# Kernel tuning notes

Measured on AMD Instinct MI355X. Metric: run time of the kernel, lower is better.

Reference implementation:

```python
import jax, jax.numpy as jnp
import numpy as np

KSIZE = 7
SIGMA = 3.0
ALPHA = 0.1
POS_VAL_FOR_ALL_NEG = 5.0
NEG_VAL_FOR_ALL_POS = -5.0


def _gauss_kernel():
    x = jnp.arange(KSIZE, dtype=jnp.float32) - (KSIZE - 1) / 2.0
    pdf = jnp.exp(-0.5 * (x / SIGMA) ** 2)
    return pdf / pdf.sum()


def _gaussian_blur(img):
    # img: (B, C, H, W); separable 7x7 gaussian, reflect padding (torchvision behavior)
    B, C, H, W = img.shape
    k = _gauss_kernel()
    pad = KSIZE // 2
    x = jnp.pad(img, ((0, 0), (0, 0), (pad, pad), (pad, pad)), mode='reflect')
    x = x.reshape(B * C, 1, H + 2 * pad, W + 2 * pad)
    kh = k.reshape(1, 1, KSIZE, 1)
    kw = k.reshape(1, 1, 1, KSIZE)
    x = jax.lax.conv_general_dilated(x, kh, (1, 1), 'VALID')
    x = jax.lax.conv_general_dilated(x, kw, (1, 1), 'VALID')
    return x.reshape(B, C, H, W)


def _dup_map(x, mask, fallback):
    # x, mask: (L,). Gather x[mask] (original order) then tile to length L.
    # Stable argsort puts True(=selected) positions first in original order.
    L = x.shape[0]
    cnt = mask.sum()
    order = jnp.argsort(jnp.logical_not(mask))  # selected indices first, stable
    idx = order[jnp.arange(L) % jnp.maximum(cnt, 1)]
    return jnp.where(cnt == 0, jnp.float32(fallback), x[idx])


_dup_vmapped = jax.vmap(_dup_map, in_axes=(0, 0, None))


def _bce_with_logits(x, y):
    # mean( max(x,0) - x*y + log1p(exp(-|x|)) ) == mean( softplus(x) - x*y )
    return jnp.mean(jnp.logaddexp(0.0, x) - x * y)


def _forward(inp, tgt):
    B, C, H, W = inp.shape
    aug_sim_target = (_gaussian_blur(tgt * 255.0) > 0).astype(jnp.float32)

    L = H * W
    x = inp.reshape(B * C, L)
    t = tgt.reshape(B * C, L)
    a = aug_sim_target.reshape(B * C, L)

    # duplicated_pos: gather input at target>0, tile; fallback +5 if no positives
    pos_mask = t > 0
    dup_pos = _dup_vmapped(x, pos_mask, POS_VAL_FOR_ALL_NEG)

    # duplicated_false_pos: prefer (input>0 & ~aug_pos); else all negatives; else -5
    aug_pos = a > 0
    fp_mask = jnp.logical_and(x > 0, jnp.logical_not(aug_pos))
    neg_mask = jnp.logical_not(aug_pos)
    cnt_fp = fp_mask.sum(axis=1, keepdims=True)
    chosen_mask = jnp.where(cnt_fp > 0, fp_mask, neg_mask)
    dup_fp = _dup_vmapped(x, chosen_mask, NEG_VAL_FOR_ALL_POS)

    sim = dup_pos * x
    aug_sim = dup_pos * dup_fp

    sim_loss = _bce_with_logits(sim, t) + _bce_with_logits(dup_pos, jnp.ones_like(x))
    aug_sim_loss = _bce_with_logits(aug_sim, jnp.zeros_like(x))
    return sim_loss + ALPHA * aug_sim_loss


def setup_inputs() -> dict:
    key = jax.random.key(0)
    k1, k2 = jax.random.split(key)
    B, C, H, W = 16, 3, 512, 512
    inp = jax.random.normal(k1, (B, C, H, W), dtype=jnp.float32)
    tgt = jax.random.randint(k2, (B, C, H, W), 0, 2).astype(jnp.float32)
    return {"input": inp, "target": tgt}


def reference(input, target):
    return _forward(input, target)
```

## Files before the change

### kernel.cpp

```cpp
#include <hip/hip_runtime.h>
#include <math.h>

constexpr int W = 512;
constexpr int HIMG = 512;
constexpr int L = 1 << 18;
constexpr int LOG2L = 18;
constexpr int TPB = 256;
constexpr int TPB1 = 512;
constexpr int TILE = 2048;
constexpr int TILES_PER_ROW = L / TILE;
constexpr int WORDS_PER_TILE = TILE / 64;
constexpr int SPB = 16;
constexpr int HALO = 3;
constexpr int HBUF = SPB + 2 * HALO;
constexpr int BLK_PER_IMG = HIMG / SPB;
constexpr int LBLK = 32;
constexpr int LOG2LBLK = 5;
constexpr int CHUNK = L / LBLK;
constexpr int LIT = CHUNK / (TPB * 4);

typedef unsigned long long ull;

__device__ __forceinline__ float softplus_f(float v) {
    return fmaxf(v, 0.0f) +
           0.6931471805599453f *
               __builtin_amdgcn_logf(1.0f + __builtin_amdgcn_exp2f(-fabsf(v) * 1.4426950408889634f));
}

__device__ __forceinline__ ull hdil7(ull prev, ull cur, ull next) {
    ull r = cur;
    r |= (cur >> 1) | (next << 63);
    r |= (cur >> 2) | (next << 62);
    r |= (cur >> 3) | (next << 61);
    r |= (cur << 1) | (prev >> 63);
    r |= (cur << 2) | (prev >> 62);
    r |= (cur << 3) | (prev >> 61);
    return r;
}

template <typename T>
__device__ __forceinline__ T sel8(const T* a, int k) {
    return k == 0 ? a[0] : k == 1 ? a[1] : k == 2 ? a[2] : k == 3 ? a[3]
         : k == 4 ? a[4] : k == 5 ? a[5] : k == 6 ? a[6] : a[7];
}

__global__ __launch_bounds__(TPB1)
void fused_mask_kernel(const float* __restrict__ x, const float* __restrict__ t,
                       ull* __restrict__ mT, ull* __restrict__ mFp, ull* __restrict__ mNeg,
                       int* __restrict__ cPos, int* __restrict__ cFp, int* __restrict__ cNeg) {
    int b = blockIdx.x;
    int img = b >> 5;
    int y0 = (b & 31) * SPB;
    int gs0 = img * HIMG + y0;

    __shared__ ull hbuf[HBUF][8];
    __shared__ ull tbuf[SPB][8];
    __shared__ ull xbuf[SPB][8];

    int lane = threadIdx.x & 63;
    int wv = threadIdx.x >> 6;
    int ylo = (y0 - HALO < 0) ? 0 : y0 - HALO;
    int yhi = (y0 + SPB - 1 + HALO > HIMG - 1) ? HIMG - 1 : y0 + SPB - 1 + HALO;

    for (int yl = ylo + wv; yl <= yhi; yl += 8) {
        int gbase = (img * HIMG + yl) * W;
        bool own = (yl >= y0) && (yl < y0 + SPB);
        ull wt[8], wx[8], h[8];
#pragma unroll
        for (int k = 0; k < 8; ++k) wt[k] = __ballot(t[gbase + k * 64 + lane] > 0.0f);
        if (own) {
#pragma unroll
            for (int k = 0; k < 8; ++k) wx[k] = __ballot(x[gbase + k * 64 + lane] > 0.0f);
        }
#pragma unroll
        for (int k = 0; k < 8; ++k) {
            ull cur = wt[k];
            ull prev = k ? wt[k - 1]
                         : ((((cur >> 1) & 1ull) << 63) | (((cur >> 2) & 1ull) << 62) |
                            (((cur >> 3) & 1ull) << 61));
            ull next = (k < 7) ? wt[k + 1]
                               : (((cur >> 62) & 1ull) | (((cur >> 61) & 1ull) << 1) |
                                  (((cur >> 60) & 1ull) << 2));
            h[k] = hdil7(prev, cur, next);
        }
        int hy = yl - (y0 - HALO);
        int k = lane & 7;
        if (lane < 8) {
            hbuf[hy][k] = sel8(h, k);
        } else if (own && lane < 16) {
            tbuf[yl - y0][k] = sel8(wt, k);
            mT[(img * HIMG + yl) * 8 + k] = sel8(wt, k);
        } else if (own && lane < 24) {
            xbuf[yl - y0][k] = sel8(wx, k);
        }
    }
    __syncthreads();

    int tid = threadIdx.x;
    if (tid < SPB * 8) {
        int ys = tid >> 3;
        int c = tid & 7;
        int y = y0 + ys;
        ull wa = 0;
#pragma unroll
        for (int d = -3; d <= 3; ++d) {
            int yy = y + d;
            yy = yy < 0 ? -yy : (yy > HIMG - 1 ? 2 * (HIMG - 1) - yy : yy);
            wa |= hbuf[yy - (y0 - HALO)][c];
        }
        ull tw = tbuf[ys][c];
        ull fp = xbuf[ys][c] & ~wa;
        ull ng = ~wa;
        int gw = gs0 * 8 + tid;
        mFp[gw] = fp;
        mNeg[gw] = ng;
        int pT = __popcll(tw), pF = __popcll(fp), pN = __popcll(ng);
#pragma unroll
        for (int m = 1; m < 32; m <<= 1) {
            pT += __shfl_xor(pT, m, 64);
            pF += __shfl_xor(pF, m, 64);
            pN += __shfl_xor(pN, m, 64);
        }
        if ((lane & 31) == 0) {
            int tile = img * TILES_PER_ROW + (y0 >> 2) + (tid >> 5);
            cPos[tile] = pT; cFp[tile] = pF; cNeg[tile] = pN;
        }
    }
}

__global__ void scan_kernel(const int* __restrict__ cPos, const int* __restrict__ cFp,
                            const int* __restrict__ cNeg,
                            int* __restrict__ oPos, int* __restrict__ oCh,
                            int* __restrict__ rCp, int* __restrict__ rCc,
                            ull* __restrict__ rMp, ull* __restrict__ rMc,
                            int* __restrict__ rUseFp) {
    int r = blockIdx.x;
    int tid = threadIdx.x;
    __shared__ int ssp[TILES_PER_ROW], ssf[TILES_PER_ROW], ssn[TILES_PER_ROW];
    int myp = cPos[r * TILES_PER_ROW + tid];
    int myf = cFp[r * TILES_PER_ROW + tid];
    int myn = cNeg[r * TILES_PER_ROW + tid];
    ssp[tid] = myp; ssf[tid] = myf; ssn[tid] = myn;
    __syncthreads();
    for (int off = 1; off < TILES_PER_ROW; off <<= 1) {
        int ap = 0, af = 0, an = 0;
        if (tid >= off) { ap = ssp[tid - off]; af = ssf[tid - off]; an = ssn[tid - off]; }
        __syncthreads();
        if (tid >= off) { ssp[tid] += ap; ssf[tid] += af; ssn[tid] += an; }
        __syncthreads();
    }
    int cp = ssp[TILES_PER_ROW - 1], cf = ssf[TILES_PER_ROW - 1], cn = ssn[TILES_PER_ROW - 1];
    bool useFp = cf > 0;
    int tile = r * TILES_PER_ROW + tid;
    oPos[tile] = ssp[tid] - myp;
    oCh[tile] = useFp ? (ssf[tid] - myf) : (ssn[tid] - myn);
    if (tid == 0) {
        int cc = useFp ? cf : cn;
        rCp[r] = cp; rCc[r] = cc; rUseFp[r] = useFp ? 1 : 0;
        ull dp_ = (ull)(cp > 0 ? cp : 1);
        ull dc_ = (ull)(cc > 0 ? cc : 1);
        rMp[r] = ((1ull << 40) + dp_ - 1) / dp_;
        rMc[r] = ((1ull << 40) + dc_ - 1) / dc_;
    }
}

__global__ __launch_bounds__(TPB)
void scatter_kernel(const float* __restrict__ x, const ull* __restrict__ mT,
                    const ull* __restrict__ mFp, const ull* __restrict__ mNeg,
                    const int* __restrict__ oPos, const int* __restrict__ oCh,
                    const int* __restrict__ rUseFp,
                    float* __restrict__ xp, float* __restrict__ xf) {
    int tile = blockIdx.x;
    int tid = threadIdx.x;
    int lane = tid & 63;
    int wv = tid >> 6;
    int r = tile >> 7;
    bool useFp = rUseFp[r] != 0;
    int widx = tile * WORDS_PER_TILE + (tid >> 3);
    int shift = (tid & 7) * 8;
    unsigned bT = (unsigned)(mT[widx] >> shift) & 0xFF;
    ull chw = useFp ? mFp[widx] : mNeg[widx];
    unsigned bCh = (unsigned)(chw >> shift) & 0xFF;
    const float4* x4 = (const float4*)x;
    int b4 = tile * (TILE / 4) + tid * 2;
    float4 a = x4[b4], b = x4[b4 + 1];
    float xv[8] = {a.x, a.y, a.z, a.w, b.x, b.y, b.z, b.w};
    int p = __popc(bT), c = __popc(bCh);
    int v = p | (c << 16);
    int incl = v;
#pragma unroll
    for (int off = 1; off < 64; off <<= 1) {
        int n = __shfl_up(incl, off, 64);
        if (lane >= off) incl += n;
    }
    __shared__ int wtot[4];
    __shared__ float bufP[TILE], bufC[TILE];
    if (lane == 63) wtot[wv] = incl;
    __syncthreads();
    int base = 0;
    if (wv > 0) base += wtot[0];
    if (wv > 1) base += wtot[1];
    if (wv > 2) base += wtot[2];
    int tot = wtot[0] + wtot[1] + wtot[2] + wtot[3];
    int excl = base + incl - v;
    int ep = excl & 0xFFFF;
    int ec = (excl >> 16) & 0xFFFF;
#pragma unroll
    for (int e = 0; e < 8; ++e) {
        if ((bT >> e) & 1) bufP[ep++] = xv[e];
        if ((bCh >> e) & 1) bufC[ec++] = xv[e];
    }
    __syncthreads();
    int P = tot & 0xFFFF, C = (tot >> 16) & 0xFFFF;
    int rL = r << LOG2L;
    int pbase = rL + oPos[tile];
    for (int i = tid; i < P; i += TPB) xp[pbase + i] = bufP[i];
    int cbase = rL + oCh[tile];
    for (int i = tid; i < C; i += TPB) xf[cbase + i] = bufC[i];
}

__global__ __launch_bounds__(TPB)
void loss_kernel(const float* __restrict__ x, const ull* __restrict__ mT,
                 const float* __restrict__ xp, const float* __restrict__ xf,
                 const int* __restrict__ rCp, const int* __restrict__ rCc,
                 const ull* __restrict__ rMp, const ull* __restrict__ rMc,
                 double* __restrict__ partial) {
    int r = blockIdx.x >> LOG2LBLK;
    int cb = (blockIdx.x & (LBLK - 1)) * CHUNK;
    int rL = r << LOG2L;
    int cp = rCp[r], cc = rCc[r];
    ull Mp = rMp[r], Mc = rMc[r];
    const float4* x4 = (const float4*)(x + rL + cb);
    const float* xpr = xp + rL;
    const float* xfr = xf + rL;
    const ull* mtr = mT + (rL >> 6);
    float local = 0.0f;
#pragma unroll
    for (int it = 0; it < LIT; ++it) {
        int o4 = it * TPB + threadIdx.x;
        unsigned l = (unsigned)(cb + (o4 << 2));
        float4 xv = x4[o4];
        unsigned tb = (unsigned)(mtr[l >> 6] >> (l & 63)) & 0xFu;
        float dps[4], dfs[4];
        if (cp > 0) {
            unsigned d = (unsigned)cp;
            unsigned q = (unsigned)(((ull)l * Mp) >> 40);
            unsigned m0 = l - q * d;
            if ((int)m0 <= (int)d - 4) {
                float4 v;
                __builtin_memcpy(&v, xpr + m0, 16);
                dps[0] = v.x; dps[1] = v.y; dps[2] = v.z; dps[3] = v.w;
            } else {
                unsigned m1 = m0 + 1; if (m1 == d) m1 = 0;
                unsigned m2 = m1 + 1; if (m2 == d) m2 = 0;
                unsigned m3 = m2 + 1; if (m3 == d) m3 = 0;
                dps[0] = xpr[m0]; dps[1] = xpr[m1]; dps[2] = xpr[m2]; dps[3] = xpr[m3];
            }
        } else {
            dps[0] = dps[1] = dps[2] = dps[3] = 5.0f;
        }
        if (cc > 0) {
            unsigned d = (unsigned)cc;
            unsigned q = (unsigned)(((ull)l * Mc) >> 40);
            unsigned m0 = l - q * d;
            if ((int)m0 <= (int)d - 4) {
                float4 v;
                __builtin_memcpy(&v, xfr + m0, 16);
                dfs[0] = v.x; dfs[1] = v.y; dfs[2] = v.z; dfs[3] = v.w;
            } else {
                unsigned m1 = m0 + 1; if (m1 == d) m1 = 0;
                unsigned m2 = m1 + 1; if (m2 == d) m2 = 0;
                unsigned m3 = m2 + 1; if (m3 == d) m3 = 0;
                dfs[0] = xfr[m0]; dfs[1] = xfr[m1]; dfs[2] = xfr[m2]; dfs[3] = xfr[m3];
            }
        } else {
            dfs[0] = dfs[1] = dfs[2] = dfs[3] = -5.0f;
        }
        float xs[4] = {xv.x, xv.y, xv.z, xv.w};
#pragma unroll
        for (int k = 0; k < 4; ++k) {
            float sim = dps[k] * xs[k];
            float s1 = ((tb >> k) & 1) ? -sim : sim;
            local += softplus_f(s1) + softplus_f(-dps[k]) + 0.1f * softplus_f(dps[k] * dfs[k]);
        }
    }
    __shared__ double sd[TPB];
    int tid = threadIdx.x;
    sd[tid] = (double)local;
    __syncthreads();
    for (int off = TPB / 2; off > 0; off >>= 1) {
        if (tid < off) sd[tid] += sd[tid + off];
        __syncthreads();
    }
    if (tid == 0) partial[blockIdx.x] = sd[0];
}

__global__ __launch_bounds__(TPB)
void final_reduce(const double* __restrict__ partial, int n,
                  float* __restrict__ out, double inv_ntot) {
    __shared__ double sd[TPB];
    double s = 0.0;
    for (int i = threadIdx.x; i < n; i += TPB) s += partial[i];
    sd[threadIdx.x] = s;
    __syncthreads();
    for (int off = TPB / 2; off > 0; off >>= 1) {
        if (threadIdx.x < off) sd[threadIdx.x] += sd[threadIdx.x + off];
        __syncthreads();
    }
    if (threadIdx.x == 0) out[0] = (float)(sd[0] * inv_ntot);
}

extern "C" void kernel_launch(void* const* d_in, const int* in_sizes, int n_in,
                              void* d_out, int out_size, void* d_ws, size_t ws_size,
                              hipStream_t stream) {
    const float* x = (const float*)d_in[0];
    const float* t = (const float*)d_in[1];
    float* out = (float*)d_out;

    int ntot = in_sizes[0];
    int R = ntot >> LOG2L;
    int numTiles = ntot / TILE;
    int nwords = ntot / 64;
    int nMaskBlk = ntot / (SPB * W);
    int nLossBlk = R * LBLK;

    char* ws = (char*)d_ws;
    size_t off = 0;
    auto alloc = [&](size_t bytes) {
        size_t p = off;
        off = (off + bytes + 255) & ~(size_t)255;
        return (void*)(ws + p);
    };
    ull* mT   = (ull*)alloc((size_t)nwords * 8);
    ull* mFp  = (ull*)alloc((size_t)nwords * 8);
    ull* mNeg = (ull*)alloc((size_t)nwords * 8);
    int* cPos = (int*)alloc(numTiles * sizeof(int));
    int* cFp  = (int*)alloc(numTiles * sizeof(int));
    int* cNeg = (int*)alloc(numTiles * sizeof(int));
    int* oPos = (int*)alloc(numTiles * sizeof(int));
    int* oCh  = (int*)alloc(numTiles * sizeof(int));
    int* rCp = (int*)alloc(R * sizeof(int));
    int* rCc = (int*)alloc(R * sizeof(int));
    int* rUseFp = (int*)alloc(R * sizeof(int));
    ull* rMp = (ull*)alloc(R * sizeof(ull));
    ull* rMc = (ull*)alloc(R * sizeof(ull));
    double* partial = (double*)alloc((size_t)nLossBlk * sizeof(double));
    float* xp = (float*)alloc((size_t)ntot * sizeof(float));
    float* xf = (float*)alloc((size_t)ntot * sizeof(float));

    fused_mask_kernel<<<nMaskBlk, TPB1, 0, stream>>>(x, t, mT, mFp, mNeg, cPos, cFp, cNeg);
    scan_kernel<<<R, TILES_PER_ROW, 0, stream>>>(cPos, cFp, cNeg, oPos, oCh,
                                                 rCp, rCc, rMp, rMc, rUseFp);
    scatter_kernel<<<numTiles, TPB, 0, stream>>>(x, mT, mFp, mNeg, oPos, oCh, rUseFp, xp, xf);
    loss_kernel<<<nLossBlk, TPB, 0, stream>>>(x, mT, xp, xf, rCp, rCc, rMp, rMc, partial);
    final_reduce<<<1, TPB, 0, stream>>>(partial, nLossBlk, out, 1.0 / (double)ntot);
}
```

Before: 160.8 us.

## Fold per-row scan into scatter and loss kernels, drop scan launch

Removes the separate scan kernel. Each scatter block now recomputes its row's exclusive tile offsets and the fp-vs-neg choice from the 128 per-tile counts using wave shuffles. Each loss block likewise recomputes the row totals and magic divisors. This saves one launch and its intermediate buffers, at the cost of redundant small reductions in every block. The positive scatter write is also vectorised to 16-byte stores where possible, although the global destination may not be 16-byte aligned.

```diff
diff --git a/kernel.cpp b/kernel.cpp
--- a/kernel.cpp
+++ b/kernel.cpp
@@ -128,54 +128,46 @@
     }
 }
 
-__global__ void scan_kernel(const int* __restrict__ cPos, const int* __restrict__ cFp,
-                            const int* __restrict__ cNeg,
-                            int* __restrict__ oPos, int* __restrict__ oCh,
-                            int* __restrict__ rCp, int* __restrict__ rCc,
-                            ull* __restrict__ rMp, ull* __restrict__ rMc,
-                            int* __restrict__ rUseFp) {
-    int r = blockIdx.x;
-    int tid = threadIdx.x;
-    __shared__ int ssp[TILES_PER_ROW], ssf[TILES_PER_ROW], ssn[TILES_PER_ROW];
-    int myp = cPos[r * TILES_PER_ROW + tid];
-    int myf = cFp[r * TILES_PER_ROW + tid];
-    int myn = cNeg[r * TILES_PER_ROW + tid];
-    ssp[tid] = myp; ssf[tid] = myf; ssn[tid] = myn;
-    __syncthreads();
-    for (int off = 1; off < TILES_PER_ROW; off <<= 1) {
-        int ap = 0, af = 0, an = 0;
-        if (tid >= off) { ap = ssp[tid - off]; af = ssf[tid - off]; an = ssn[tid - off]; }
-        __syncthreads();
-        if (tid >= off) { ssp[tid] += ap; ssf[tid] += af; ssn[tid] += an; }
-        __syncthreads();
-    }
-    int cp = ssp[TILES_PER_ROW - 1], cf = ssf[TILES_PER_ROW - 1], cn = ssn[TILES_PER_ROW - 1];
-    bool useFp = cf > 0;
-    int tile = r * TILES_PER_ROW + tid;
-    oPos[tile] = ssp[tid] - myp;
-    oCh[tile] = useFp ? (ssf[tid] - myf) : (ssn[tid] - myn);
-    if (tid == 0) {
-        int cc = useFp ? cf : cn;
-        rCp[r] = cp; rCc[r] = cc; rUseFp[r] = useFp ? 1 : 0;
-        ull dp_ = (ull)(cp > 0 ? cp : 1);
-        ull dc_ = (ull)(cc > 0 ? cc : 1);
-        rMp[r] = ((1ull << 40) + dp_ - 1) / dp_;
-        rMc[r] = ((1ull << 40) + dc_ - 1) / dc_;
-    }
-}
-
 __global__ __launch_bounds__(TPB)
 void scatter_kernel(const float* __restrict__ x, const ull* __restrict__ mT,
                     const ull* __restrict__ mFp, const ull* __restrict__ mNeg,
-                    const int* __restrict__ oPos, const int* __restrict__ oCh,
-                    const int* __restrict__ rUseFp,
+                    const int* __restrict__ cPos, const int* __restrict__ cFp,
+                    const int* __restrict__ cNeg,
                     float* __restrict__ xp, float* __restrict__ xf) {
     int tile = blockIdx.x;
     int tid = threadIdx.x;
     int lane = tid & 63;
     int wv = tid >> 6;
     int r = tile >> 7;
-    bool useFp = rUseFp[r] != 0;
+    int tIdx = tile & 127;
+    int rowbase = r * TILES_PER_ROW;
+
+    int cpj = 0, cfj = 0, cnj = 0;
+    if (tid < TILES_PER_ROW) {
+        cpj = cPos[rowbase + tid];
+        cfj = cFp[rowbase + tid];
+        cnj = cNeg[rowbase + tid];
+    }
+    int totf = cfj;
+    int prep = (tid < tIdx) ? cpj : 0;
+    int pref = (tid < tIdx) ? cfj : 0;
+    int pren = (tid < tIdx) ? cnj : 0;
+#pragma unroll
+    for (int m = 1; m < 64; m <<= 1) {
+        totf += __shfl_xor(totf, m, 64);
+        prep += __shfl_xor(prep, m, 64);
+        pref += __shfl_xor(pref, m, 64);
+        pren += __shfl_xor(pren, m, 64);
+    }
+    __shared__ int red[4][4];
+    if (lane == 0) { red[wv][0] = totf; red[wv][1] = prep; red[wv][2] = pref; red[wv][3] = pren; }
+    __syncthreads();
+    int totF  = red[0][0] + red[1][0] + red[2][0] + red[3][0];
+    int oPosv = red[0][1] + red[1][1] + red[2][1] + red[3][1];
+    bool useFp = totF > 0;
+    int oChv = useFp ? (red[0][2] + red[1][2] + red[2][2] + red[3][2])
+                     : (red[0][3] + red[1][3] + red[2][3] + red[3][3]);
+
     int widx = tile * WORDS_PER_TILE + (tid >> 3);
     int shift = (tid & 7) * 8;
     unsigned bT = (unsigned)(mT[widx] >> shift) & 0xFF;
@@ -194,7 +186,8 @@
         if (lane >= off) incl += n;
     }
     __shared__ int wtot[4];
-    __shared__ float bufP[TILE], bufC[TILE];
+    __shared__ __align__(16) float bufP[TILE];
+    __shared__ __align__(16) float bufC[TILE];
     if (lane == 63) wtot[wv] = incl;
     __syncthreads();
     int base = 0;
@@ -213,23 +206,61 @@
     __syncthreads();
     int P = tot & 0xFFFF, C = (tot >> 16) & 0xFFFF;
     int rL = r << LOG2L;
-    int pbase = rL + oPos[tile];
-    for (int i = tid; i < P; i += TPB) xp[pbase + i] = bufP[i];
-    int cbase = rL + oCh[tile];
+    int pbase = rL + oPosv;
+    int P4 = P & ~3;
+    for (int i = tid * 4; i < P4; i += TPB * 4)
+        __builtin_memcpy(&xp[pbase + i], &bufP[i], 16);
+    for (int i = P4 + tid; i < P; i += TPB) xp[pbase + i] = bufP[i];
+    int cbase = rL + oChv;
     for (int i = tid; i < C; i += TPB) xf[cbase + i] = bufC[i];
 }
 
 __global__ __launch_bounds__(TPB)
 void loss_kernel(const float* __restrict__ x, const ull* __restrict__ mT,
                  const float* __restrict__ xp, const float* __restrict__ xf,
-                 const int* __restrict__ rCp, const int* __restrict__ rCc,
-                 const ull* __restrict__ rMp, const ull* __restrict__ rMc,
+                 const int* __restrict__ cPos, const int* __restrict__ cFp,
+                 const int* __restrict__ cNeg,
                  double* __restrict__ partial) {
     int r = blockIdx.x >> LOG2LBLK;
     int cb = (blockIdx.x & (LBLK - 1)) * CHUNK;
     int rL = r << LOG2L;
-    int cp = rCp[r], cc = rCc[r];
-    ull Mp = rMp[r], Mc = rMc[r];
+    int tid = threadIdx.x;
+    int lane = tid & 63;
+    int wv = tid >> 6;
+    int rowbase = r * TILES_PER_ROW;
+
+    int ap = 0, af = 0, an = 0;
+    if (tid < TILES_PER_ROW) {
+        ap = cPos[rowbase + tid];
+        af = cFp[rowbase + tid];
+        an = cNeg[rowbase + tid];
+    }
+#pragma unroll
+    for (int m = 1; m < 64; m <<= 1) {
+        ap += __shfl_xor(ap, m, 64);
+        af += __shfl_xor(af, m, 64);
+        an += __shfl_xor(an, m, 64);
+    }
+    __shared__ int red[4][3];
+    __shared__ int sCp, sCc;
+    __shared__ ull sMp, sMc;
+    if (lane == 0) { red[wv][0] = ap; red[wv][1] = af; red[wv][2] = an; }
+    __syncthreads();
+    if (tid == 0) {
+        int cp_ = red[0][0] + red[1][0] + red[2][0] + red[3][0];
+        int cf_ = red[0][1] + red[1][1] + red[2][1] + red[3][1];
+        int cn_ = red[0][2] + red[1][2] + red[2][2] + red[3][2];
+        int cc_ = cf_ > 0 ? cf_ : cn_;
+        sCp = cp_; sCc = cc_;
+        ull dp_ = (ull)(cp_ > 0 ? cp_ : 1);
+        ull dc_ = (ull)(cc_ > 0 ? cc_ : 1);
+        sMp = ((1ull << 40) + dp_ - 1) / dp_;
+        sMc = ((1ull << 40) + dc_ - 1) / dc_;
+    }
+    __syncthreads();
+    int cp = sCp, cc = sCc;
+    ull Mp = sMp, Mc = sMc;
+
     const float4* x4 = (const float4*)(x + rL + cb);
     const float* xpr = xp + rL;
     const float* xfr = xf + rL;
@@ -237,7 +268,7 @@
     float local = 0.0f;
 #pragma unroll
     for (int it = 0; it < LIT; ++it) {
-        int o4 = it * TPB + threadIdx.x;
+        int o4 = it * TPB + tid;
         unsigned l = (unsigned)(cb + (o4 << 2));
         float4 xv = x4[o4];
         unsigned tb = (unsigned)(mtr[l >> 6] >> (l & 63)) & 0xFu;
@@ -285,7 +316,6 @@
         }
     }
     __shared__ double sd[TPB];
-    int tid = threadIdx.x;
     sd[tid] = (double)local;
     __syncthreads();
     for (int off = TPB / 2; off > 0; off >>= 1) {
@@ -337,21 +367,12 @@
     int* cPos = (int*)alloc(numTiles * sizeof(int));
     int* cFp  = (int*)alloc(numTiles * sizeof(int));
     int* cNeg = (int*)alloc(numTiles * sizeof(int));
-    int* oPos = (int*)alloc(numTiles * sizeof(int));
-    int* oCh  = (int*)alloc(numTiles * sizeof(int));
-    int* rCp = (int*)alloc(R * sizeof(int));
-    int* rCc = (int*)alloc(R * sizeof(int));
-    int* rUseFp = (int*)alloc(R * sizeof(int));
-    ull* rMp = (ull*)alloc(R * sizeof(ull));
-    ull* rMc = (ull*)alloc(R * sizeof(ull));
     double* partial = (double*)alloc((size_t)nLossBlk * sizeof(double));
     float* xp = (float*)alloc((size_t)ntot * sizeof(float));
     float* xf = (float*)alloc((size_t)ntot * sizeof(float));
 
     fused_mask_kernel<<<nMaskBlk, TPB1, 0, stream>>>(x, t, mT, mFp, mNeg, cPos, cFp, cNeg);
-    scan_kernel<<<R, TILES_PER_ROW, 0, stream>>>(cPos, cFp, cNeg, oPos, oCh,
-                                                 rCp, rCc, rMp, rMc, rUseFp);
-    scatter_kernel<<<numTiles, TPB, 0, stream>>>(x, mT, mFp, mNeg, oPos, oCh, rUseFp, xp, xf);
-    loss_kernel<<<nLossBlk, TPB, 0, stream>>>(x, mT, xp, xf, rCp, rCc, rMp, rMc, partial);
+    scatter_kernel<<<numTiles, TPB, 0, stream>>>(x, mT, mFp, mNeg, cPos, cFp, cNeg, xp, xf);
+    loss_kernel<<<nLossBlk, TPB, 0, stream>>>(x, mT, xp, xf, cPos, cFp, cNeg, partial);
     final_reduce<<<1, TPB, 0, stream>>>(partial, nLossBlk, out, 1.0 / (double)ntot);
 }
```

After: 165.6 us. 1.03x slower.
